# Kernel optimization log

Measured on AMD Instinct MI355X. Metric: run time of the kernel, lower is better.

## Reference

```python
import jax, jax.numpy as jnp
import numpy as np

N = 50000        # nodes
E = 800000       # edges (avg degree 16)
NODE_D = 128     # node_attr_dim
EDGE_D = 16      # edge_attr_dim
HID = 300        # hidden_dim (module default)


def setup_inputs() -> dict:
    key = jax.random.key(0)
    ks = jax.random.split(key, 8)
    x = jax.random.normal(ks[0], (N, NODE_D), jnp.float32)
    edge_attr = jax.random.normal(ks[1], (E, EDGE_D), jnp.float32)
    edge_weight = jax.random.uniform(ks[2], (E,), jnp.float32)
    node_weight = jax.random.uniform(ks[3], (N,), jnp.float32)
    edge_index = jax.random.randint(ks[4], (2, E), 0, N, jnp.int32)
    # lin0: Linear(node_attr_dim + edge_attr_dim, hidden_dim)
    W0 = jax.random.normal(ks[5], (NODE_D + EDGE_D, HID), jnp.float32) / np.sqrt(NODE_D + EDGE_D)
    b0 = jnp.zeros((HID,), jnp.float32)
    # mp_layer.linear: Linear(hidden_dim, hidden_dim)
    W = jax.random.normal(ks[6], (HID, HID), jnp.float32) / np.sqrt(HID)
    b = jnp.zeros((HID,), jnp.float32)
    return dict(x=x, edge_attr=edge_attr, edge_weight=edge_weight,
                node_weight=node_weight, W0=W0, b0=b0, W=W, b=b,
                edge_index=edge_index)


def reference(x, edge_attr, edge_weight, node_weight, W0, b0, W, b, edge_index):
    src = edge_index[0]   # x_j (source, flow='source_to_target')
    dst = edge_index[1]   # aggregation target i
    n = x.shape[0]

    # --- isFirstLayer: weighted sum of incoming edge features, scattered at dst ---
    inc = jax.ops.segment_sum(edge_weight[:, None] * edge_attr, dst, num_segments=n)  # [N, EDGE_D]
    h0 = jax.nn.relu(jnp.concatenate([x, inc], axis=1) @ W0 + b0)                     # [N, HID]

    # --- MessagePassingLayer: message = edge_weight * x_j; aggr = mean at dst ---
    msg = edge_weight[:, None] * h0[src]                                              # [E, HID]
    agg = jax.ops.segment_sum(msg, dst, num_segments=n)                               # [N, HID]
    deg = jax.ops.segment_sum(jnp.ones((src.shape[0],), x.dtype), dst, num_segments=n)
    agg = agg / jnp.maximum(deg, 1.0)[:, None]  # scatter-mean (0 where no incoming edges)

    # --- update: relu(h0 + linear(aggr)) (add_residual=True) ---
    h = jax.nn.relu(h0 + agg @ W + b)
    # isLastLayer=False -> no node_weight scaling
    return (h, h0)
```

## Files before the change

### kernel.cpp

```cpp
#include <hip/hip_runtime.h>

#define NN 50000
#define NE 800000
#define ND 128
#define ED 16
#define HID 300
#define KP1 192
#define KP2 320
#define NP 320

#define SCAN_T 256
#define SCAN_B ((NN + SCAN_T - 1) / SCAN_T)

typedef __attribute__((ext_vector_type(8))) short short8;
typedef __attribute__((ext_vector_type(4))) float f32x4;

__device__ __forceinline__ unsigned short f2b(float f) {
    unsigned int u = __float_as_uint(f);
    u = (u + 0x7FFFu + ((u >> 16) & 1u)) >> 16;
    return (unsigned short)u;
}
__device__ __forceinline__ float blo(unsigned int u) {
    return __uint_as_float(u << 16);
}
__device__ __forceinline__ float bhi(unsigned int u) {
    return __uint_as_float(u & 0xffff0000u);
}

__device__ __forceinline__ void gload16(const void* g, void* l) {
    __builtin_amdgcn_global_load_lds(
        (const __attribute__((address_space(1))) void*)g,
        (__attribute__((address_space(3))) void*)l, 16, 0, 0);
}

__device__ __forceinline__ int block_iscan(int v, int tid) {
    int lane = tid & 63;
    #pragma unroll
    for (int off = 1; off < 64; off <<= 1) {
        int t = __shfl_up(v, off);
        if (lane >= off) v += t;
    }
    __shared__ int wsum[4];
    int wid = tid >> 6;
    if (lane == 63) wsum[wid] = v;
    __syncthreads();
    int add = 0;
    #pragma unroll
    for (int w = 0; w < 4; ++w)
        if (w < wid) add += wsum[w];
    return v + add;
}

__global__ void hist_kernel(const int* __restrict__ ei, int* __restrict__ rowptr) {
    int e4 = (blockIdx.x * blockDim.x + threadIdx.x) * 4;
    if (e4 < NE) {
        int4 d = *(const int4*)&ei[NE + e4];
        atomicAdd(&rowptr[d.x + 1], 1);
        atomicAdd(&rowptr[d.y + 1], 1);
        atomicAdd(&rowptr[d.z + 1], 1);
        atomicAdd(&rowptr[d.w + 1], 1);
    }
}

__global__ __launch_bounds__(SCAN_T) void scan1(int* __restrict__ rowptr,
                                                int* __restrict__ blockSums) {
    int i = blockIdx.x * SCAN_T + threadIdx.x;
    int v = (i < NN) ? rowptr[1 + i] : 0;
    v = block_iscan(v, threadIdx.x);
    if (i < NN) rowptr[1 + i] = v;
    if (threadIdx.x == SCAN_T - 1) blockSums[blockIdx.x] = v;
}

__global__ __launch_bounds__(SCAN_T) void scan2(int* __restrict__ blockSums) {
    int t = threadIdx.x;
    int orig = (t < SCAN_B) ? blockSums[t] : 0;
    int v = block_iscan(orig, t);
    if (t < SCAN_B) blockSums[t] = v - orig;
}

__global__ __launch_bounds__(SCAN_T) void scan3(int* __restrict__ rowptr,
                                                const int* __restrict__ blockSums,
                                                int* __restrict__ cursor) {
    int i = blockIdx.x * SCAN_T + threadIdx.x;
    if (i < NN) {
        int v = rowptr[1 + i] + blockSums[blockIdx.x];
        rowptr[1 + i] = v;
        if (i + 1 < NN) cursor[i + 1] = v;
    }
    if (i == 0) cursor[0] = 0;
}

__global__ void fill_kernel(const int* __restrict__ ei, const float* __restrict__ ew,
                            int* __restrict__ cursor, uint4* __restrict__ csr) {
    int e = blockIdx.x * blockDim.x + threadIdx.x;
    if (e < NE) {
        int d = ei[NE + e];
        int pos = atomicAdd(&cursor[d], 1);
        uint4 q;
        q.x = (unsigned int)ei[e];
        q.y = (unsigned int)e;
        q.z = __float_as_uint(ew[e]);
        q.w = 0;
        csr[pos] = q;
    }
}

__global__ __launch_bounds__(256) void prep_kernel(
    const float* __restrict__ x,
    const float* __restrict__ edge_attr,
    const int* __restrict__ rowptr,
    const uint4* __restrict__ csr,
    unsigned short* __restrict__ A1) {
    int n = (blockIdx.x * blockDim.x + threadIdx.x) >> 6;
    int lane = threadIdx.x & 63;
    if (n >= NN) return;

    float2 v = *(const float2*)&x[(size_t)n * ND + lane * 2];
    unsigned int o = (unsigned int)f2b(v.x) | ((unsigned int)f2b(v.y) << 16);
    *(unsigned int*)&A1[(size_t)n * KP1 + lane * 2] = o;

    int g = lane >> 4, j = lane & 15;
    int lo = rowptr[n], hi = rowptr[n + 1];
    float s = 0.f;
    for (int k = lo + g; k < hi; k += 16) {
        int k1 = (k + 4  < hi) ? k + 4  : k;
        int k2 = (k + 8  < hi) ? k + 8  : k;
        int k3 = (k + 12 < hi) ? k + 12 : k;
        uint4 e0 = csr[k],  e1 = csr[k1];
        uint4 e2 = csr[k2], e3 = csr[k3];
        float a0 = edge_attr[(size_t)e0.y * ED + j];
        float a1 = edge_attr[(size_t)e1.y * ED + j];
        float a2 = edge_attr[(size_t)e2.y * ED + j];
        float a3 = edge_attr[(size_t)e3.y * ED + j];
        s += __uint_as_float(e0.z) * a0;
        s += ((k + 4  < hi) ? __uint_as_float(e1.z) : 0.f) * a1;
        s += ((k + 8  < hi) ? __uint_as_float(e2.z) : 0.f) * a2;
        s += ((k + 12 < hi) ? __uint_as_float(e3.z) : 0.f) * a3;
    }
    s += __shfl_xor(s, 16);
    s += __shfl_xor(s, 32);
    if (lane < 16)
        A1[(size_t)n * KP1 + ND + lane] = f2b(s);
    else
        A1[(size_t)n * KP1 + ND + lane] = 0;
}

__global__ void castB0(const float* __restrict__ W0, unsigned short* __restrict__ B0T) {
    int n = blockIdx.x, k = threadIdx.x;
    float v = (n < HID && k < ND + ED) ? W0[(size_t)k * HID + n] : 0.f;
    B0T[(size_t)n * KP1 + k] = f2b(v);
}

__global__ void castB(const float* __restrict__ W, unsigned short* __restrict__ BT) {
    int n = blockIdx.x, k = threadIdx.x;
    float v = (n < HID && k < HID) ? W[(size_t)k * HID + n] : 0.f;
    BT[(size_t)n * KP2 + k] = f2b(v);
}

template <int MODE, int KP, int BN, int WM, int WN, int RPB, int THR>
__global__ __launch_bounds__(THR) void gemm_stream(
    const unsigned short* __restrict__ A,
    const unsigned short* __restrict__ BT,
    const float* __restrict__ bias,
    const float* __restrict__ RES,
    float* __restrict__ C,
    unsigned short* __restrict__ h0b,
    int M)
{
    constexpr int CPR = KP / 8;
    constexpr int ACH = 32 * CPR;
    constexpr int BCH = BN * CPR;
    constexpr int NW  = THR / 64;
    constexpr int AM  = 32 / (16 * WM);
    constexpr int BNW = BN / (16 * WN);
    static_assert(WM * WN == NW, "wave grid must cover block");
    __shared__ unsigned short Bs[BCH * 8];
    __shared__ unsigned short As[2][ACH * 8];

    const int tid = threadIdx.x;
    const int wave = tid >> 6, lane = tid & 63;
    const int wm = wave / WN, wn = wave % WN;
    const int quad = lane >> 4, lr = lane & 15;
    const int n00 = blockIdx.y * BN;
    const int ncol = n00 + wn * (BNW * 16);
    const int rbase = blockIdx.x * RPB;
    const int rowend = min(rbase + RPB, M);
    const int nt = (rowend - rbase + 31) >> 5;

    auto stageA = [&](int buf, int mb) {
        for (int s = tid; s < ACH; s += THR) {
            int row = s / CPR, c = s - row * CPR;
            int cs = (c & ~7) | ((c & 7) ^ (row & 7));
            int mg = mb + row; if (mg >= M) mg = M - 1;
            gload16(&A[(size_t)mg * KP + cs * 8], &As[buf][s * 8]);
        }
    };

    for (int s = tid; s < BCH; s += THR) {
        int row = s / CPR, c = s - row * CPR;
        int cs = (c & ~7) | ((c & 7) ^ (row & 7));
        gload16(&BT[(size_t)(n00 + row) * KP + cs * 8], &Bs[s * 8]);
    }
    stageA(0, rbase);

    float bias_r[BNW];
    #pragma unroll
    for (int tn = 0; tn < BNW; ++tn) {
        int ng = ncol + tn * 16 + lr;
        bias_r[tn] = (ng < HID) ? bias[ng] : 0.f;
    }
    __syncthreads();

    int cur = 0;
    #pragma unroll 1
    for (int t = 0; t < nt; ++t) {
        const int mb = rbase + t * 32;
        if (t + 1 < nt) stageA(cur ^ 1, mb + 32);

        float res_r[AM][BNW][4];
        if (MODE == 1) {
            #pragma unroll
            for (int tm = 0; tm < AM; ++tm)
            #pragma unroll
            for (int tn = 0; tn < BNW; ++tn) {
                int ng = ncol + tn * 16 + lr;
                int ngc = ng < HID ? ng : HID - 1;
                #pragma unroll
                for (int r = 0; r < 4; ++r) {
                    int mg = mb + (wm * AM + tm) * 16 + quad * 4 + r;
                    int mgc = mg < M ? mg : M - 1;
                    res_r[tm][tn][r] = RES[(size_t)mgc * HID + ngc];
                }
            }
        }

        f32x4 acc[AM][BNW] = {};
        const int rm = lr & 7;
        #pragma unroll
        for (int tt = 0; tt < KP / 32; ++tt) {
            int cA = tt * 4 + quad;
            int sw8 = ((cA & ~7) | ((cA & 7) ^ rm)) * 8;
            short8 a[AM], b[BNW];
            #pragma unroll
            for (int tm = 0; tm < AM; ++tm) {
                int ar = (wm * AM + tm) * 16 + lr;
                a[tm] = *(const short8*)&As[cur][ar * KP + sw8];
            }
            #pragma unroll
            for (int tn = 0; tn < BNW; ++tn) {
                int br = wn * (BNW * 16) + tn * 16 + lr;
                b[tn] = *(const short8*)&Bs[br * KP + sw8];
            }
            #pragma unroll
            for (int tm = 0; tm < AM; ++tm)
                #pragma unroll
                for (int tn = 0; tn < BNW; ++tn)
                    acc[tm][tn] = __builtin_amdgcn_mfma_f32_16x16x32_bf16(
                        a[tm], b[tn], acc[tm][tn], 0, 0, 0);
        }

        #pragma unroll
        for (int tm = 0; tm < AM; ++tm)
        #pragma unroll
        for (int tn = 0; tn < BNW; ++tn) {
            int ng = ncol + tn * 16 + lr;
            #pragma unroll
            for (int r = 0; r < 4; ++r) {
                int mg = mb + (wm * AM + tm) * 16 + quad * 4 + r;
                if (mg < rowend && ng < HID) {
                    float v = acc[tm][tn][r] + bias_r[tn];
                    if (MODE == 1) v += res_r[tm][tn][r];
                    v = fmaxf(v, 0.f);
                    C[(size_t)mg * HID + ng] = v;
                    if (MODE == 0) h0b[(size_t)mg * NP + ng] = f2b(v);
                }
            }
        }
        __syncthreads();
        cur ^= 1;
    }
}

__device__ __forceinline__ void acc8(float* acc, float w, const uint4& r) {
    acc[0] += w * blo(r.x); acc[1] += w * bhi(r.x);
    acc[2] += w * blo(r.y); acc[3] += w * bhi(r.y);
    acc[4] += w * blo(r.z); acc[5] += w * bhi(r.z);
    acc[6] += w * blo(r.w); acc[7] += w * bhi(r.w);
}

__global__ __launch_bounds__(256) void agg_kernel(
    const unsigned short* __restrict__ h0b,
    const int* __restrict__ rowptr,
    const uint4* __restrict__ csr,
    unsigned short* __restrict__ aggB)
{
    int n = (blockIdx.x * blockDim.x + threadIdx.x) >> 6;
    int lane = threadIdx.x & 63;
    if (n >= NN) return;
    int lo = rowptr[n], hi = rowptr[n + 1];
    float acc[8] = {};
    const uint4* h4 = (const uint4*)h0b;
    bool act = lane < 40;
    for (int k = lo; k < hi; k += 4) {
        uint4 p0 = csr[k];
        uint4 p1 = csr[(k + 1 < hi) ? k + 1 : k];
        uint4 p2 = csr[(k + 2 < hi) ? k + 2 : k];
        uint4 p3 = csr[(k + 3 < hi) ? k + 3 : k];
        float w0 = __uint_as_float(p0.z);
        float w1 = (k + 1 < hi) ? __uint_as_float(p1.z) : 0.f;
        float w2 = (k + 2 < hi) ? __uint_as_float(p2.z) : 0.f;
        float w3 = (k + 3 < hi) ? __uint_as_float(p3.z) : 0.f;
        uint4 r0 = {0,0,0,0}, r1 = {0,0,0,0}, r2 = {0,0,0,0}, r3 = {0,0,0,0};
        if (act) {
            r0 = h4[(size_t)p0.x * 40 + lane];
            r1 = h4[(size_t)p1.x * 40 + lane];
            r2 = h4[(size_t)p2.x * 40 + lane];
            r3 = h4[(size_t)p3.x * 40 + lane];
        }
        acc8(acc, w0, r0); acc8(acc, w1, r1);
        acc8(acc, w2, r2); acc8(acc, w3, r3);
    }
    if (act) {
        float invd = 1.f / fmaxf((float)(hi - lo), 1.f);
        int cbase = lane * 8;
        unsigned int o[4];
        #pragma unroll
        for (int i = 0; i < 4; ++i) {
            int c0 = cbase + 2 * i, c1 = c0 + 1;
            unsigned int ulo = (c0 < HID) ? f2b(acc[2 * i] * invd) : 0;
            unsigned int uhi = (c1 < HID) ? f2b(acc[2 * i + 1] * invd) : 0;
            o[i] = ulo | (uhi << 16);
        }
        uint4* a4 = (uint4*)aggB;
        uint4 v; v.x = o[0]; v.y = o[1]; v.z = o[2]; v.w = o[3];
        a4[(size_t)n * 40 + lane] = v;
    }
}

extern "C" void kernel_launch(void* const* d_in, const int* in_sizes, int n_in,
                              void* d_out, int out_size, void* d_ws, size_t ws_size,
                              hipStream_t stream) {
    const float* x           = (const float*)d_in[0];
    const float* edge_attr   = (const float*)d_in[1];
    const float* edge_weight = (const float*)d_in[2];
    const float* W0 = (const float*)d_in[4];
    const float* b0 = (const float*)d_in[5];
    const float* W  = (const float*)d_in[6];
    const float* b  = (const float*)d_in[7];
    const int* ei   = (const int*)d_in[8];

    float* out = (float*)d_out;
    float* h  = out;
    float* h0 = out + (size_t)NN * HID;

    char* p = (char*)d_ws;
    auto alloc = [&](size_t bytes) { char* q = p; p += (bytes + 255) & ~(size_t)255; return q; };
    int*   rowptr  = (int*)  alloc((NN + 1) * sizeof(int));
    int*   cursor  = (int*)  alloc(NN * sizeof(int));
    int*   bsums   = (int*)  alloc(SCAN_B * sizeof(int));
    uint4* csr     = (uint4*)alloc((size_t)NE * sizeof(uint4));
    unsigned short* A1   = (unsigned short*)alloc((size_t)NN * KP1 * 2);
    unsigned short* h0b  = (unsigned short*)alloc((size_t)NN * NP * 2);
    unsigned short* aggB = (unsigned short*)alloc((size_t)NN * NP * 2);
    unsigned short* B0T  = (unsigned short*)alloc((size_t)NP * KP1 * 2);
    unsigned short* BT   = (unsigned short*)alloc((size_t)NP * KP2 * 2);

    hipMemsetAsync(rowptr, 0, (NN + 1) * sizeof(int), stream);
    hist_kernel<<<(NE / 4 + 255) / 256, 256, 0, stream>>>(ei, rowptr);
    scan1<<<SCAN_B, SCAN_T, 0, stream>>>(rowptr, bsums);
    scan2<<<1, SCAN_T, 0, stream>>>(bsums);
    scan3<<<SCAN_B, SCAN_T, 0, stream>>>(rowptr, bsums, cursor);
    fill_kernel<<<(NE + 255) / 256, 256, 0, stream>>>(ei, edge_weight, cursor, csr);
    castB0<<<NP, KP1, 0, stream>>>(W0, B0T);
    castB<<<NP, KP2, 0, stream>>>(W, BT);
    prep_kernel<<<(NN + 3) / 4, 256, 0, stream>>>(x, edge_attr, rowptr, csr, A1);

    gemm_stream<0, KP1, 320, 2, 4, 196, 512><<<dim3(256, 1), 512, 0, stream>>>(
        A1, B0T, b0, nullptr, h0, h0b, NN);
    agg_kernel<<<(NN + 3) / 4, 256, 0, stream>>>(h0b, rowptr, csr, aggB);
    gemm_stream<1, KP2, 160, 2, 2, 391, 256><<<dim3(128, 2), 256, 0, stream>>>(
        aggB, BT, b, h0, h, nullptr, NN);
}
```

Baseline: 442.5 us.

## Compute incoming edge-feature sum with atomics and shrink CSR entries to 8 bytes

Replaces the CSR-based gather of edge_attr in prep_kernel with a separate kernel that does a float atomicAdd per edge and feature into a zeroed per-node accumulator. The edge id is then no longer needed in the CSR, so each entry shrinks from 16 to 8 bytes, halving CSR write and read traffic in fill and aggregation. The cost is 12.8M float atomics plus an extra memset, and the atomic accumulation order is nondeterministic.

```diff
diff --git a/kernel.cpp b/kernel.cpp
--- a/kernel.cpp
+++ b/kernel.cpp
@@ -62,6 +62,18 @@
     }
 }
 
+__global__ __launch_bounds__(256) void inc_atomic(
+    const int* __restrict__ ei, const float* __restrict__ ew,
+    const float* __restrict__ edge_attr, float* __restrict__ incacc) {
+    int t = blockIdx.x * blockDim.x + threadIdx.x;
+    int e = t >> 4, j = t & 15;
+    if (e < NE) {
+        int d = ei[NE + e];
+        float w = ew[e];
+        atomicAdd(&incacc[(size_t)d * ED + j], w * edge_attr[(size_t)e * ED + j]);
+    }
+}
+
 __global__ __launch_bounds__(SCAN_T) void scan1(int* __restrict__ rowptr,
                                                 int* __restrict__ blockSums) {
     int i = blockIdx.x * SCAN_T + threadIdx.x;
@@ -91,25 +103,21 @@
 }
 
 __global__ void fill_kernel(const int* __restrict__ ei, const float* __restrict__ ew,
-                            int* __restrict__ cursor, uint4* __restrict__ csr) {
+                            int* __restrict__ cursor, uint2* __restrict__ csr) {
     int e = blockIdx.x * blockDim.x + threadIdx.x;
     if (e < NE) {
         int d = ei[NE + e];
         int pos = atomicAdd(&cursor[d], 1);
-        uint4 q;
+        uint2 q;
         q.x = (unsigned int)ei[e];
-        q.y = (unsigned int)e;
-        q.z = __float_as_uint(ew[e]);
-        q.w = 0;
+        q.y = __float_as_uint(ew[e]);
         csr[pos] = q;
     }
 }
 
 __global__ __launch_bounds__(256) void prep_kernel(
     const float* __restrict__ x,
-    const float* __restrict__ edge_attr,
-    const int* __restrict__ rowptr,
-    const uint4* __restrict__ csr,
+    const float* __restrict__ incacc,
     unsigned short* __restrict__ A1) {
     int n = (blockIdx.x * blockDim.x + threadIdx.x) >> 6;
     int lane = threadIdx.x & 63;
@@ -119,30 +127,9 @@
     unsigned int o = (unsigned int)f2b(v.x) | ((unsigned int)f2b(v.y) << 16);
     *(unsigned int*)&A1[(size_t)n * KP1 + lane * 2] = o;
 
-    int g = lane >> 4, j = lane & 15;
-    int lo = rowptr[n], hi = rowptr[n + 1];
-    float s = 0.f;
-    for (int k = lo + g; k < hi; k += 16) {
-        int k1 = (k + 4  < hi) ? k + 4  : k;
-        int k2 = (k + 8  < hi) ? k + 8  : k;
-        int k3 = (k + 12 < hi) ? k + 12 : k;
-        uint4 e0 = csr[k],  e1 = csr[k1];
-        uint4 e2 = csr[k2], e3 = csr[k3];
-        float a0 = edge_attr[(size_t)e0.y * ED + j];
-        float a1 = edge_attr[(size_t)e1.y * ED + j];
-        float a2 = edge_attr[(size_t)e2.y * ED + j];
-        float a3 = edge_attr[(size_t)e3.y * ED + j];
-        s += __uint_as_float(e0.z) * a0;
-        s += ((k + 4  < hi) ? __uint_as_float(e1.z) : 0.f) * a1;
-        s += ((k + 8  < hi) ? __uint_as_float(e2.z) : 0.f) * a2;
-        s += ((k + 12 < hi) ? __uint_as_float(e3.z) : 0.f) * a3;
-    }
-    s += __shfl_xor(s, 16);
-    s += __shfl_xor(s, 32);
-    if (lane < 16)
-        A1[(size_t)n * KP1 + ND + lane] = f2b(s);
-    else
-        A1[(size_t)n * KP1 + ND + lane] = 0;
+    unsigned short ov = 0;
+    if (lane < ED) ov = f2b(incacc[(size_t)n * ED + lane]);
+    A1[(size_t)n * KP1 + ND + lane] = ov;
 }
 
 __global__ void castB0(const float* __restrict__ W0, unsigned short* __restrict__ B0T) {
@@ -291,7 +278,7 @@
 __global__ __launch_bounds__(256) void agg_kernel(
     const unsigned short* __restrict__ h0b,
     const int* __restrict__ rowptr,
-    const uint4* __restrict__ csr,
+    const uint2* __restrict__ csr,
     unsigned short* __restrict__ aggB)
 {
     int n = (blockIdx.x * blockDim.x + threadIdx.x) >> 6;
@@ -302,14 +289,14 @@
     const uint4* h4 = (const uint4*)h0b;
     bool act = lane < 40;
     for (int k = lo; k < hi; k += 4) {
-        uint4 p0 = csr[k];
-        uint4 p1 = csr[(k + 1 < hi) ? k + 1 : k];
-        uint4 p2 = csr[(k + 2 < hi) ? k + 2 : k];
-        uint4 p3 = csr[(k + 3 < hi) ? k + 3 : k];
-        float w0 = __uint_as_float(p0.z);
-        float w1 = (k + 1 < hi) ? __uint_as_float(p1.z) : 0.f;
-        float w2 = (k + 2 < hi) ? __uint_as_float(p2.z) : 0.f;
-        float w3 = (k + 3 < hi) ? __uint_as_float(p3.z) : 0.f;
+        uint2 p0 = csr[k];
+        uint2 p1 = csr[(k + 1 < hi) ? k + 1 : k];
+        uint2 p2 = csr[(k + 2 < hi) ? k + 2 : k];
+        uint2 p3 = csr[(k + 3 < hi) ? k + 3 : k];
+        float w0 = __uint_as_float(p0.y);
+        float w1 = (k + 1 < hi) ? __uint_as_float(p1.y) : 0.f;
+        float w2 = (k + 2 < hi) ? __uint_as_float(p2.y) : 0.f;
+        float w3 = (k + 3 < hi) ? __uint_as_float(p3.y) : 0.f;
         uint4 r0 = {0,0,0,0}, r1 = {0,0,0,0}, r2 = {0,0,0,0}, r3 = {0,0,0,0};
         if (act) {
             r0 = h4[(size_t)p0.x * 40 + lane];
@@ -358,7 +345,8 @@
     int*   rowptr  = (int*)  alloc((NN + 1) * sizeof(int));
     int*   cursor  = (int*)  alloc(NN * sizeof(int));
     int*   bsums   = (int*)  alloc(SCAN_B * sizeof(int));
-    uint4* csr     = (uint4*)alloc((size_t)NE * sizeof(uint4));
+    float* incacc  = (float*)alloc((size_t)NN * ED * sizeof(float));
+    uint2* csr     = (uint2*)alloc((size_t)NE * sizeof(uint2));
     unsigned short* A1   = (unsigned short*)alloc((size_t)NN * KP1 * 2);
     unsigned short* h0b  = (unsigned short*)alloc((size_t)NN * NP * 2);
     unsigned short* aggB = (unsigned short*)alloc((size_t)NN * NP * 2);
@@ -366,14 +354,16 @@
     unsigned short* BT   = (unsigned short*)alloc((size_t)NP * KP2 * 2);
 
     hipMemsetAsync(rowptr, 0, (NN + 1) * sizeof(int), stream);
+    hipMemsetAsync(incacc, 0, (size_t)NN * ED * sizeof(float), stream);
     hist_kernel<<<(NE / 4 + 255) / 256, 256, 0, stream>>>(ei, rowptr);
+    inc_atomic<<<NE * 16 / 256, 256, 0, stream>>>(ei, edge_weight, edge_attr, incacc);
     scan1<<<SCAN_B, SCAN_T, 0, stream>>>(rowptr, bsums);
     scan2<<<1, SCAN_T, 0, stream>>>(bsums);
     scan3<<<SCAN_B, SCAN_T, 0, stream>>>(rowptr, bsums, cursor);
     fill_kernel<<<(NE + 255) / 256, 256, 0, stream>>>(ei, edge_weight, cursor, csr);
     castB0<<<NP, KP1, 0, stream>>>(W0, B0T);
     castB<<<NP, KP2, 0, stream>>>(W, BT);
-    prep_kernel<<<(NN + 3) / 4, 256, 0, stream>>>(x, edge_attr, rowptr, csr, A1);
+    prep_kernel<<<(NN + 3) / 4, 256, 0, stream>>>(x, incacc, A1);
 
     gemm_stream<0, KP1, 320, 2, 4, 196, 512><<<dim3(256, 1), 512, 0, stream>>>(
         A1, B0T, b0, nullptr, h0, h0b, NN);
```

New measurement: 448.3 us. About the same (+1.3%).
